# Performance work log

Measured on AMD Instinct MI355X. Metric: run time of the kernel, lower is better.

Reference implementation:

```python
import jax, jax.numpy as jnp
import numpy as np

B, L, I, H = 64, 512, 512, 768


def _lstm_dir(x, W_ih, W_hh, b, h0, c0):
    # x: (B, L, I); W_ih: (4H, I); W_hh: (4H, H); b: (4H,); h0, c0: (B, H)
    # Precompute input projection for all timesteps (big dense GEMM).
    xg = jnp.einsum('bli,gi->lbg', x, W_ih) + b  # (L, B, 4H)

    def step(carry, xg_t):
        h, c = carry
        gates = xg_t + h @ W_hh.T  # (B, 4H)
        i, f, g, o = jnp.split(gates, 4, axis=-1)
        i = jax.nn.sigmoid(i)
        f = jax.nn.sigmoid(f)
        g = jnp.tanh(g)
        o = jax.nn.sigmoid(o)
        c = f * c + i * g
        h = o * jnp.tanh(c)
        return (h, c), h

    (h_n, c_n), hs = jax.lax.scan(step, (h0, c0), xg)
    return hs.transpose(1, 0, 2), h_n, c_n  # (B, L, H), (B, H), (B, H)


def setup_inputs() -> dict:
    key = jax.random.key(0)
    ks = jax.random.split(key, 8)
    stdv = 1.0 / np.sqrt(H)
    u = lambda k, shape: jax.random.uniform(k, shape, jnp.float32, -stdv, stdv)
    return {
        'x': jax.random.normal(ks[0], (B, L, I), jnp.float32),
        'weight_ih': u(ks[1], (4 * H, I)),
        'weight_hh': u(ks[2], (4 * H, H)),
        'bias': u(ks[3], (4 * H,)),
        'weight_ih_reverse': u(ks[4], (4 * H, I)),
        'weight_hh_reverse': u(ks[5], (4 * H, H)),
        'bias_reverse': u(ks[6], (4 * H,)),
        'h0': jnp.zeros((2, B, H), jnp.float32),
        'c0': jnp.zeros((2, B, H), jnp.float32),
    }


def reference(x, weight_ih, weight_hh, bias, weight_ih_reverse,
              weight_hh_reverse, bias_reverse, h0, c0):
    # forward direction
    out_f, hn_f, cn_f = _lstm_dir(x, weight_ih, weight_hh, bias, h0[0], c0[0])
    # reverse direction: flip time, scan, flip back
    out_r, hn_r, cn_r = _lstm_dir(x[:, ::-1, :], weight_ih_reverse,
                                  weight_hh_reverse, bias_reverse, h0[1], c0[1])
    out_r = out_r[:, ::-1, :]
    h_all = jnp.concatenate([out_f, out_r], axis=-1)  # (B, L, 2H)
    h_n = jnp.stack([hn_f, hn_r], axis=0)             # (2, B, H)
    c_n = jnp.stack([cn_f, cn_r], axis=0)             # (2, B, H)
    return h_all, h_n, c_n
```

## Files before the change

### kernel.cpp

```cpp
#include <hip/hip_runtime.h>
#include <cmath>

#define BATCH 64
#define SEQL  512
#define INDIM 512
#define HID   768
#define G4    3072
#define KTOT  1280
#define KS    10
#define KC    128
#define JB    12
#define RPB   256
#define NBLK  240
#define NTHR  256
#define E2    (2*BATCH*HID)
#define HALLN ((size_t)BATCH*SEQL*2*HID)

__device__ __forceinline__ void grid_barrier(unsigned* cnt, unsigned target) {
    __syncthreads();
    if (threadIdx.x == 0) {
        __threadfence();
        __hip_atomic_fetch_add(cnt, 1u, __ATOMIC_RELAXED, __HIP_MEMORY_SCOPE_AGENT);
        while (__hip_atomic_load(cnt, __ATOMIC_RELAXED, __HIP_MEMORY_SCOPE_AGENT) < target)
            __builtin_amdgcn_s_sleep(1);
        __threadfence();
    }
    __syncthreads();
}

__device__ __forceinline__ float sigmoidf_(float x) { return 1.0f / (1.0f + expf(-x)); }

__global__ __launch_bounds__(256) void k_transpose_x(const float* __restrict__ x,
                                                     float* __restrict__ xT) {
    __shared__ float tile[64][65];
    const int bidx = blockIdx.x;
    const int t  = bidx >> 3;
    const int kt = (bidx & 7) * 64;
    const int tid = threadIdx.x;
#pragma unroll
    for (int p = 0; p < 16; ++p) {
        int idx = p * 256 + tid;
        int b = idx >> 6, kl = idx & 63;
        tile[b][kl] = x[((size_t)b * SEQL + t) * INDIM + kt + kl];
    }
    __syncthreads();
#pragma unroll
    for (int p = 0; p < 16; ++p) {
        int idx = p * 256 + tid;
        int kl = idx >> 6, b = idx & 63;
        xT[((size_t)t * INDIM + kt + kl) * BATCH + b] = tile[b][kl];
    }
}

__global__ __launch_bounds__(256) void k_pack_w(const float* __restrict__ wih0,
                                                const float* __restrict__ whh0,
                                                const float* __restrict__ wih1,
                                                const float* __restrict__ whh1,
                                                float* __restrict__ Wt) {
    __shared__ float tile[64][65];
    const int bidx = blockIdx.x;
    const int d   = bidx / 960;
    const int rem = bidx % 960;
    const int kt  = rem / 48;
    const int rt  = rem % 48;
    const float* wih = d ? wih1 : wih0;
    const float* whh = d ? whh1 : whh0;
    const int kbase = kt * 64, rbase = rt * 64;
    const int tid = threadIdx.x;
#pragma unroll
    for (int p = 0; p < 16; ++p) {
        int idx = p * 256 + tid;
        int rl = idx >> 6, kl = idx & 63;
        int k = kbase + kl, r = rbase + rl;
        float v = (k < INDIM) ? wih[(size_t)r * INDIM + k]
                              : whh[(size_t)r * HID + (k - INDIM)];
        tile[rl][kl] = v;
    }
    __syncthreads();
#pragma unroll
    for (int p = 0; p < 16; ++p) {
        int idx = p * 256 + tid;
        int kl = idx >> 6, rl = idx & 63;
        Wt[((size_t)d * KTOT + kbase + kl) * G4 + rbase + rl] = tile[rl][kl];
    }
}

__global__ __launch_bounds__(NTHR, 2)
void k_lstm_persist(const float* __restrict__ x,   const float* __restrict__ xT, int use_xt,
                    const float* __restrict__ Wt,  int use_wt,
                    const float* __restrict__ wih0, const float* __restrict__ whh0,
                    const float* __restrict__ wih1, const float* __restrict__ whh1,
                    const float* __restrict__ bias0, const float* __restrict__ bias1,
                    const float* __restrict__ h0,   const float* __restrict__ c0,
                    float* __restrict__ out,  float* __restrict__ Gpart,
                    float* __restrict__ hT,   float* __restrict__ cbuf,
                    unsigned* __restrict__ barcnt)
{
    __shared__ float InL[32][64];
    __shared__ float WL[32][256];
    const int tid = threadIdx.x;
    const int bid = blockIdx.x;
    const int d   = bid / (JB * KS);
    const int rem = bid % (JB * KS);
    const int rb  = rem / KS;
    const int kb  = rem % KS;
    const int r0  = rb * RPB;
    const int k0  = kb * KC;
    const int tr  = tid & 31;
    const int tb  = tid >> 5;
    const int gtid = bid * NTHR + tid;
    unsigned bar = 0;

    for (int e = gtid; e < E2; e += NBLK * NTHR) {
        int b = e / (2 * HID); int rr = e % (2 * HID); int dd = rr / HID; int j = rr % HID;
        size_t src = (size_t)(dd * BATCH + b) * HID + j;
        hT[(size_t)(dd * HID + j) * BATCH + b] = h0[src];
        cbuf[src] = c0[src];
    }
    grid_barrier(barcnt, (++bar) * NBLK);

    for (int t = 0; t < SEQL; ++t) {
        const int t_eff = d ? (SEQL - 1 - t) : t;

        float acc[8][8];
#pragma unroll
        for (int i = 0; i < 8; ++i)
#pragma unroll
            for (int m = 0; m < 8; ++m) acc[i][m] = 0.0f;

        for (int kc = 0; kc < KC; kc += 32) {
            __syncthreads();
            if (k0 >= INDIM || use_xt) {
#pragma unroll
                for (int p = 0; p < 2; ++p) {
                    int idx = p * NTHR + tid;
                    int b4 = idx & 15, kr = idx >> 4;
                    int k = k0 + kc + kr;
                    const float* src = (k < INDIM)
                        ? (xT + ((size_t)t_eff * INDIM + k) * BATCH)
                        : (hT + ((size_t)d * HID + (k - INDIM)) * BATCH);
                    *(float4*)&InL[kr][b4 * 4] = *(const float4*)(src + b4 * 4);
                }
            } else {
#pragma unroll
                for (int p = 0; p < 8; ++p) {
                    int idx = p * NTHR + tid;
                    int b = idx & 63, kr = idx >> 6;
                    int k = k0 + kc + kr;
                    InL[kr][b] = x[((size_t)b * SEQL + t_eff) * INDIM + k];
                }
            }
            if (use_wt) {
                const float* wbase = Wt + (size_t)d * KTOT * G4;
#pragma unroll
                for (int p = 0; p < 8; ++p) {
                    int idx = p * NTHR + tid;
                    int f4 = idx & 63, kr = idx >> 6;
                    int k = k0 + kc + kr;
                    *(float4*)&WL[kr][f4 * 4] =
                        *(const float4*)(wbase + (size_t)k * G4 + r0 + f4 * 4);
                }
            } else {
                const float* wih = d ? wih1 : wih0;
                const float* whh = d ? whh1 : whh0;
#pragma unroll
                for (int p = 0; p < 8; ++p) {
                    int idx = p * NTHR + tid;
                    int f4 = idx & 63, kr = idx >> 6;
                    int k = k0 + kc + kr;
#pragma unroll
                    for (int m = 0; m < 4; ++m) {
                        int r = r0 + f4 * 4 + m;
                        WL[kr][f4 * 4 + m] = (k < INDIM)
                            ? wih[(size_t)r * INDIM + k]
                            : whh[(size_t)r * HID + (k - INDIM)];
                    }
                }
            }
            __syncthreads();
#pragma unroll 4
            for (int k = 0; k < 32; ++k) {
                float4 a0 = *(const float4*)&InL[k][tb * 8];
                float4 a1 = *(const float4*)&InL[k][tb * 8 + 4];
                float4 w0 = *(const float4*)&WL[k][tr * 4];
                float4 w1 = *(const float4*)&WL[k][128 + tr * 4];
                float av[8] = {a0.x, a0.y, a0.z, a0.w, a1.x, a1.y, a1.z, a1.w};
                float wv[8] = {w0.x, w0.y, w0.z, w0.w, w1.x, w1.y, w1.z, w1.w};
#pragma unroll
                for (int bi = 0; bi < 8; ++bi)
#pragma unroll
                    for (int m = 0; m < 8; ++m)
                        acc[bi][m] = fmaf(av[bi], wv[m], acc[bi][m]);
            }
        }
        {
            float* gp = Gpart + (size_t)(d * KS + kb) * ((size_t)BATCH * G4);
#pragma unroll
            for (int bi = 0; bi < 8; ++bi) {
                float* row = gp + (size_t)(tb * 8 + bi) * G4 + r0;
                *(float4*)(row + tr * 4) =
                    make_float4(acc[bi][0], acc[bi][1], acc[bi][2], acc[bi][3]);
                *(float4*)(row + 128 + tr * 4) =
                    make_float4(acc[bi][4], acc[bi][5], acc[bi][6], acc[bi][7]);
            }
        }
        grid_barrier(barcnt, (++bar) * NBLK);

        for (int e = gtid; e < E2; e += NBLK * NTHR) {
            int b = e / (2 * HID); int rr = e % (2 * HID); int dd = rr / HID; int j = rr % HID;
            const float* bs = dd ? bias1 : bias0;
            float gv[4];
#pragma unroll
            for (int gi = 0; gi < 4; ++gi) {
                int row = gi * HID + j;
                float s = bs[row];
#pragma unroll
                for (int q = 0; q < KS; ++q)
                    s += Gpart[(size_t)(dd * KS + q) * ((size_t)BATCH * G4) + (size_t)b * G4 + row];
                gv[gi] = s;
            }
            float ig = sigmoidf_(gv[0]);
            float fg = sigmoidf_(gv[1]);
            float gg = tanhf(gv[2]);
            float og = sigmoidf_(gv[3]);
            size_t ci = (size_t)(dd * BATCH + b) * HID + j;
            float cn = fg * cbuf[ci] + ig * gg;
            cbuf[ci] = cn;
            float hn = og * tanhf(cn);
            hT[(size_t)(dd * HID + j) * BATCH + b] = hn;
            int t_out = dd ? (SEQL - 1 - t) : t;
            out[((size_t)b * SEQL + t_out) * (2 * HID) + dd * HID + j] = hn;
            if (t == SEQL - 1) {
                out[HALLN + ci] = hn;
                out[HALLN + E2 + ci] = cn;
            }
        }
        grid_barrier(barcnt, (++bar) * NBLK);
    }
}

extern "C" void kernel_launch(void* const* d_in, const int* in_sizes, int n_in,
                              void* d_out, int out_size, void* d_ws, size_t ws_size,
                              hipStream_t stream) {
    const float* x     = (const float*)d_in[0];
    const float* wih0  = (const float*)d_in[1];
    const float* whh0  = (const float*)d_in[2];
    const float* bias0 = (const float*)d_in[3];
    const float* wih1  = (const float*)d_in[4];
    const float* whh1  = (const float*)d_in[5];
    const float* bias1 = (const float*)d_in[6];
    const float* h0    = (const float*)d_in[7];
    const float* c0    = (const float*)d_in[8];
    float* out = (float*)d_out;
    float* ws  = (float*)d_ws;

    size_t off = 0;
    float* Gpart = ws + off; off += (size_t)2 * KS * BATCH * G4;
    float* hT    = ws + off; off += (size_t)2 * HID * BATCH;
    float* cbuf  = ws + off; off += (size_t)2 * BATCH * HID;
    unsigned* barcnt = (unsigned*)(ws + off); off += 64;
    float* Wt = ws + off;
    size_t off_wt = off + (size_t)2 * KTOT * G4;
    float* xT = ws + off_wt;
    size_t off_xt = off_wt + (size_t)SEQL * INDIM * BATCH;
    int use_wt = (ws_size >= off_wt * sizeof(float)) ? 1 : 0;
    int use_xt = (ws_size >= off_xt * sizeof(float)) ? 1 : 0;

    hipMemsetAsync(barcnt, 0, 256, stream);
    if (use_wt) k_pack_w<<<1920, 256, 0, stream>>>(wih0, whh0, wih1, whh1, Wt);
    if (use_xt) k_transpose_x<<<4096, 256, 0, stream>>>(x, xT);

    k_lstm_persist<<<NBLK, NTHR, 0, stream>>>(
        x, xT, use_xt, Wt, use_wt,
        wih0, whh0, wih1, whh1, bias0, bias1, h0, c0,
        out, Gpart, hT, cbuf, barcnt);
}
```

Before: 46.03 ms.

## Keep per-block weight slice resident in LDS across all timesteps

The persistent LSTM kernel now loads each block's weight slice (128 K-rows by 128 gate rows) into LDS once before the time loop, instead of re-streaming weights from global memory every timestep. To fit, the grid doubles to 480 blocks, each owning 128 gate rows, and the per-thread tile shrinks to 8x4. Input/hidden tiles are staged in LDS in 64-row chunks through dynamic shared memory, with a fallback variant that reads them directly from global memory if the large LDS allocation is refused. The trade-off is 480 blocks joining every grid barrier and roughly 80KB of LDS per block, which limits residency; if all 480 blocks cannot be co-resident, the spin barrier deadlocks.

Measured after the change: 66.69 ms. +44.9%, slower.

```diff
diff --git a/kernel.cpp b/kernel.cpp
--- a/kernel.cpp
+++ b/kernel.cpp
@@ -9,9 +9,9 @@
 #define KTOT  1280
 #define KS    10
 #define KC    128
-#define JB    12
-#define RPB   256
-#define NBLK  240
+#define JB    24
+#define RPB   128
+#define NBLK  480
 #define NTHR  256
 #define E2    (2*BATCH*HID)
 #define HALLN ((size_t)BATCH*SEQL*2*HID)
@@ -33,9 +33,8 @@
 __global__ __launch_bounds__(256) void k_transpose_x(const float* __restrict__ x,
                                                      float* __restrict__ xT) {
     __shared__ float tile[64][65];
-    const int bidx = blockIdx.x;
-    const int t  = bidx >> 3;
-    const int kt = (bidx & 7) * 64;
+    const int t  = blockIdx.x >> 3;
+    const int kt = (blockIdx.x & 7) * 64;
     const int tid = threadIdx.x;
 #pragma unroll
     for (int p = 0; p < 16; ++p) {
@@ -58,9 +57,8 @@
                                                 const float* __restrict__ whh1,
                                                 float* __restrict__ Wt) {
     __shared__ float tile[64][65];
-    const int bidx = blockIdx.x;
-    const int d   = bidx / 960;
-    const int rem = bidx % 960;
+    const int d   = blockIdx.x / 960;
+    const int rem = blockIdx.x % 960;
     const int kt  = rem / 48;
     const int rt  = rem % 48;
     const float* wih = d ? wih1 : wih0;
@@ -72,9 +70,8 @@
         int idx = p * 256 + tid;
         int rl = idx >> 6, kl = idx & 63;
         int k = kbase + kl, r = rbase + rl;
-        float v = (k < INDIM) ? wih[(size_t)r * INDIM + k]
-                              : whh[(size_t)r * HID + (k - INDIM)];
-        tile[rl][kl] = v;
+        tile[rl][kl] = (k < INDIM) ? wih[(size_t)r * INDIM + k]
+                                   : whh[(size_t)r * HID + (k - INDIM)];
     }
     __syncthreads();
 #pragma unroll
@@ -85,6 +82,7 @@
     }
 }
 
+template <int INL>
 __global__ __launch_bounds__(NTHR, 2)
 void k_lstm_persist(const float* __restrict__ x,   const float* __restrict__ xT, int use_xt,
                     const float* __restrict__ Wt,  int use_wt,
@@ -96,8 +94,10 @@
                     float* __restrict__ hT,   float* __restrict__ cbuf,
                     unsigned* __restrict__ barcnt)
 {
-    __shared__ float InL[32][64];
-    __shared__ float WL[32][256];
+    extern __shared__ float smem[];
+    float* WL  = smem;
+    float* InL = smem + KC * RPB;
+
     const int tid = threadIdx.x;
     const int bid = blockIdx.x;
     const int d   = bid / (JB * KS);
@@ -111,6 +111,28 @@
     const int gtid = bid * NTHR + tid;
     unsigned bar = 0;
 
+    if (use_wt) {
+        const float* wbase = Wt + (size_t)d * KTOT * G4;
+#pragma unroll
+        for (int p = 0; p < 16; ++p) {
+            int idx = p * NTHR + tid;
+            int f4 = idx & 31, kl = idx >> 5;
+            *(float4*)&WL[kl * RPB + f4 * 4] =
+                *(const float4*)(wbase + (size_t)(k0 + kl) * G4 + r0 + f4 * 4);
+        }
+    } else {
+        const float* wih = d ? wih1 : wih0;
+        const float* whh = d ? whh1 : whh0;
+        for (int p = 0; p < 64; ++p) {
+            int idx = p * NTHR + tid;
+            int r = idx & 127, kl = idx >> 7;
+            int k = k0 + kl;
+            WL[kl * RPB + r] = (k < INDIM)
+                ? wih[(size_t)(r0 + r) * INDIM + k]
+                : whh[(size_t)(r0 + r) * HID + (k - INDIM)];
+        }
+    }
+
     for (int e = gtid; e < E2; e += NBLK * NTHR) {
         int b = e / (2 * HID); int rr = e % (2 * HID); int dd = rr / HID; int j = rr % HID;
         size_t src = (size_t)(dd * BATCH + b) * HID + j;
@@ -122,87 +144,82 @@
     for (int t = 0; t < SEQL; ++t) {
         const int t_eff = d ? (SEQL - 1 - t) : t;
 
-        float acc[8][8];
+        float acc[8][4];
 #pragma unroll
         for (int i = 0; i < 8; ++i)
 #pragma unroll
-            for (int m = 0; m < 8; ++m) acc[i][m] = 0.0f;
-
-        for (int kc = 0; kc < KC; kc += 32) {
-            __syncthreads();
-            if (k0 >= INDIM || use_xt) {
-#pragma unroll
-                for (int p = 0; p < 2; ++p) {
-                    int idx = p * NTHR + tid;
-                    int b4 = idx & 15, kr = idx >> 4;
-                    int k = k0 + kc + kr;
-                    const float* src = (k < INDIM)
-                        ? (xT + ((size_t)t_eff * INDIM + k) * BATCH)
-                        : (hT + ((size_t)d * HID + (k - INDIM)) * BATCH);
-                    *(float4*)&InL[kr][b4 * 4] = *(const float4*)(src + b4 * 4);
+            for (int m = 0; m < 4; ++m) acc[i][m] = 0.0f;
+
+#pragma unroll
+        for (int c = 0; c < 2; ++c) {
+            const int kc0 = k0 + c * 64;
+            const float* src64 = (kc0 < INDIM)
+                ? (use_xt ? xT + ((size_t)t_eff * INDIM + kc0) * BATCH : nullptr)
+                : (hT + ((size_t)d * HID + (kc0 - INDIM)) * BATCH);
+
+            if (INL) {
+                __syncthreads();
+                if (src64) {
+#pragma unroll
+                    for (int p = 0; p < 4; ++p) {
+                        int idx = p * NTHR + tid;
+                        int b4 = idx & 15, kr = idx >> 4;
+                        *(float4*)&InL[kr * BATCH + b4 * 4] =
+                            *(const float4*)(src64 + (size_t)kr * BATCH + b4 * 4);
+                    }
+                } else {
+#pragma unroll
+                    for (int p = 0; p < 16; ++p) {
+                        int idx = p * NTHR + tid;
+                        int b = idx & 63, kr = idx >> 6;
+                        InL[kr * BATCH + b] =
+                            x[((size_t)b * SEQL + t_eff) * INDIM + kc0 + kr];
+                    }
+                }
+                __syncthreads();
+#pragma unroll 8
+                for (int k = 0; k < 64; ++k) {
+                    float4 w = *(const float4*)&WL[(c * 64 + k) * RPB + tr * 4];
+                    float4 a0 = *(const float4*)&InL[k * BATCH + tb * 8];
+                    float4 a1 = *(const float4*)&InL[k * BATCH + tb * 8 + 4];
+                    float av[8] = {a0.x, a0.y, a0.z, a0.w, a1.x, a1.y, a1.z, a1.w};
+                    float wv[4] = {w.x, w.y, w.z, w.w};
+#pragma unroll
+                    for (int bi = 0; bi < 8; ++bi)
+#pragma unroll
+                        for (int m = 0; m < 4; ++m)
+                            acc[bi][m] = fmaf(av[bi], wv[m], acc[bi][m]);
                 }
             } else {
-#pragma unroll
-                for (int p = 0; p < 8; ++p) {
-                    int idx = p * NTHR + tid;
-                    int b = idx & 63, kr = idx >> 6;
-                    int k = k0 + kc + kr;
-                    InL[kr][b] = x[((size_t)b * SEQL + t_eff) * INDIM + k];
+#pragma unroll 4
+                for (int k = 0; k < 64; ++k) {
+                    float4 w = *(const float4*)&WL[(c * 64 + k) * RPB + tr * 4];
+                    float av[8];
+                    if (src64) {
+                        float4 a0 = *(const float4*)(src64 + (size_t)k * BATCH + tb * 8);
+                        float4 a1 = *(const float4*)(src64 + (size_t)k * BATCH + tb * 8 + 4);
+                        av[0]=a0.x; av[1]=a0.y; av[2]=a0.z; av[3]=a0.w;
+                        av[4]=a1.x; av[5]=a1.y; av[6]=a1.z; av[7]=a1.w;
+                    } else {
+#pragma unroll
+                        for (int bi = 0; bi < 8; ++bi)
+                            av[bi] = x[((size_t)(tb * 8 + bi) * SEQL + t_eff) * INDIM + kc0 + k];
+                    }
+                    float wv[4] = {w.x, w.y, w.z, w.w};
+#pragma unroll
+                    for (int bi = 0; bi < 8; ++bi)
+#pragma unroll
+                        for (int m = 0; m < 4; ++m)
+                            acc[bi][m] = fmaf(av[bi], wv[m], acc[bi][m]);
                 }
             }
-            if (use_wt) {
-                const float* wbase = Wt + (size_t)d * KTOT * G4;
-#pragma unroll
-                for (int p = 0; p < 8; ++p) {
-                    int idx = p * NTHR + tid;
-                    int f4 = idx & 63, kr = idx >> 6;
-                    int k = k0 + kc + kr;
-                    *(float4*)&WL[kr][f4 * 4] =
-                        *(const float4*)(wbase + (size_t)k * G4 + r0 + f4 * 4);
-                }
-            } else {
-                const float* wih = d ? wih1 : wih0;
-                const float* whh = d ? whh1 : whh0;
-#pragma unroll
-                for (int p = 0; p < 8; ++p) {
-                    int idx = p * NTHR + tid;
-                    int f4 = idx & 63, kr = idx >> 6;
-                    int k = k0 + kc + kr;
-#pragma unroll
-                    for (int m = 0; m < 4; ++m) {
-                        int r = r0 + f4 * 4 + m;
-                        WL[kr][f4 * 4 + m] = (k < INDIM)
-                            ? wih[(size_t)r * INDIM + k]
-                            : whh[(size_t)r * HID + (k - INDIM)];
-                    }
-                }
-            }
-            __syncthreads();
-#pragma unroll 4
-            for (int k = 0; k < 32; ++k) {
-                float4 a0 = *(const float4*)&InL[k][tb * 8];
-                float4 a1 = *(const float4*)&InL[k][tb * 8 + 4];
-                float4 w0 = *(const float4*)&WL[k][tr * 4];
-                float4 w1 = *(const float4*)&WL[k][128 + tr * 4];
-                float av[8] = {a0.x, a0.y, a0.z, a0.w, a1.x, a1.y, a1.z, a1.w};
-                float wv[8] = {w0.x, w0.y, w0.z, w0.w, w1.x, w1.y, w1.z, w1.w};
-#pragma unroll
-                for (int bi = 0; bi < 8; ++bi)
-#pragma unroll
-                    for (int m = 0; m < 8; ++m)
-                        acc[bi][m] = fmaf(av[bi], wv[m], acc[bi][m]);
-            }
         }
         {
             float* gp = Gpart + (size_t)(d * KS + kb) * ((size_t)BATCH * G4);
 #pragma unroll
-            for (int bi = 0; bi < 8; ++bi) {
-                float* row = gp + (size_t)(tb * 8 + bi) * G4 + r0;
-                *(float4*)(row + tr * 4) =
+            for (int bi = 0; bi < 8; ++bi)
+                *(float4*)(gp + (size_t)(tb * 8 + bi) * G4 + r0 + tr * 4) =
                     make_float4(acc[bi][0], acc[bi][1], acc[bi][2], acc[bi][3]);
-                *(float4*)(row + 128 + tr * 4) =
-                    make_float4(acc[bi][4], acc[bi][5], acc[bi][6], acc[bi][7]);
-            }
         }
         grid_barrier(barcnt, (++bar) * NBLK);
 
@@ -270,8 +287,21 @@
     if (use_wt) k_pack_w<<<1920, 256, 0, stream>>>(wih0, whh0, wih1, whh1, Wt);
     if (use_xt) k_transpose_x<<<4096, 256, 0, stream>>>(x, xT);
 
-    k_lstm_persist<<<NBLK, NTHR, 0, stream>>>(
-        x, xT, use_xt, Wt, use_wt,
-        wih0, whh0, wih1, whh1, bias0, bias1, h0, c0,
-        out, Gpart, hT, cbuf, barcnt);
-}
+    static int inl_mode = -1;
+    if (inl_mode < 0) {
+        hipError_t e = hipFuncSetAttribute(
+            reinterpret_cast<const void*>(&k_lstm_persist<1>),
+            hipFuncAttributeMaxDynamicSharedMemorySize, (KC * RPB + 64 * BATCH) * 4);
+        inl_mode = (e == hipSuccess) ? 1 : 0;
+    }
+
+    if (inl_mode) {
+        k_lstm_persist<1><<<NBLK, NTHR, (KC * RPB + 64 * BATCH) * 4, stream>>>(
+            x, xT, use_xt, Wt, use_wt, wih0, whh0, wih1, whh1, bias0, bias1,
+            h0, c0, out, Gpart, hT, cbuf, barcnt);
+    } else {
+        k_lstm_persist<0><<<NBLK, NTHR, KC * RPB * 4, stream>>>(
+            x, xT, use_xt, Wt, use_wt, wih0, whh0, wih1, whh1, bias0, bias1,
+            h0, c0, out, Gpart, hT, cbuf, barcnt);
+    }
+}
```
